# Kernel optimization log

Measured on AMD Instinct MI355X. Metric: run time of the kernel, lower is better.

The kernel has to match this reference:

```python
import jax, jax.numpy as jnp
import numpy as np

NUM_HEADS = 8


def setup_inputs() -> dict:
    B, S, D, Q, SEG = 4, 4096, 512, 1, 256
    key = jax.random.key(0)
    ks = jax.random.split(key, 7)
    x = jax.random.normal(ks[0], (B, S, D), dtype=jnp.float32)
    seg_id = jnp.sort(jax.random.randint(ks[1], (B, S), 0, SEG), axis=-1)
    # ensure every row actually spans segment ids 0..SEG-1 so max()+1 == SEG
    seg_id = seg_id.at[:, 0].set(0).at[:, -1].set(SEG - 1)
    valid_mask = jnp.ones((B, S), dtype=bool)
    query_bank = jax.random.normal(ks[2], (1, 1, Q, D), dtype=jnp.float32)
    scale = 0.02
    w_q = jax.random.normal(ks[3], (D, D), dtype=jnp.float32) * scale
    w_k = jax.random.normal(ks[4], (D, D), dtype=jnp.float32) * scale
    w_v = jax.random.normal(ks[5], (D, D), dtype=jnp.float32) * scale
    w_o = jax.random.normal(ks[6], (D, D), dtype=jnp.float32) * scale
    return {"x": x, "seg_id": seg_id, "valid_mask": valid_mask, "s_seg_max": SEG,
            "query_bank": query_bank, "w_q": w_q, "w_k": w_k, "w_v": w_v, "w_o": w_o}


def reference(x, seg_id, valid_mask, s_seg_max, query_bank, w_q, w_k, w_v, w_o):
    B, S, D = x.shape
    Q = query_bank.shape[2]
    H = NUM_HEADS
    hd = D // H
    L = s_seg_max * Q  # number of pooled queries

    # expand learned query bank over batch and segments, project (Linear: x @ W.T)
    queries = jnp.broadcast_to(query_bank, (B, s_seg_max, Q, D)).reshape(B, L, D)
    q = (queries @ w_q.T).reshape(B, L, H, hd).transpose(0, 2, 1, 3)   # bhqd
    k = (x @ w_k.T).reshape(B, S, H, hd).transpose(0, 2, 1, 3)         # bhkd
    v = (x @ w_v.T).reshape(B, S, H, hd).transpose(0, 2, 1, 3)         # bhkd

    # torch SDPA boolean mask semantics: True = participate in attention
    seg_for_query = jnp.repeat(jnp.arange(s_seg_max), Q)               # [L]
    attend = (seg_id[:, None, :] != seg_for_query[None, :, None]) | (~valid_mask[:, None, :])  # [B,L,S]

    scores = jnp.einsum('bhqd,bhkd->bhqk', q, k) / np.sqrt(hd).astype(x.dtype)
    scores = jnp.where(attend[:, None, :, :], scores, -jnp.inf)
    attn = jax.nn.softmax(scores, axis=-1)
    out = jnp.einsum('bhqk,bhkd->bhqd', attn, v)                       # [B,H,L,hd]
    out = out.transpose(0, 2, 1, 3).reshape(B, L, D)
    return out @ w_o.T
```

## Files before the change

kernel.cpp:

```cpp
#include <hip/hip_runtime.h>
#include <hip/hip_bf16.h>


#define S 4096
#define D 512
#define H 8
#define SEG 256
#define NROW 1024

typedef short bf16x8 __attribute__((ext_vector_type(8)));
typedef float fvec4  __attribute__((ext_vector_type(4)));

constexpr int OFF_SEGO   = 0;
constexpr int OFF_DSEG   = 1032;
constexpr int OFF_NALL   = 9224;
constexpr int OFF_C16    = 11272;
constexpr int OFF_PSEG_F = 15368;
constexpr int OFF_NSEG_F = 2112520;
constexpr size_t WS_FLOATS = 2374664;

static __device__ inline ushort f2bf(float f) {
    __hip_bfloat16 h = __float2bfloat16(f);
    return *reinterpret_cast<ushort*>(&h);
}
static __device__ inline float bf2f(ushort u) {
    return __uint_as_float(((uint)u) << 16);
}
static __device__ inline uint pack2(float a, float b) {
    return (uint)f2bf(a) | ((uint)f2bf(b) << 16);
}

__global__ __launch_bounds__(512) void k_setup(const float* __restrict__ qb,
        const float* __restrict__ w_q, const float* __restrict__ w_k,
        const int* __restrict__ seg_id, float* __restrict__ W) {
    int tid = threadIdx.x, blk = blockIdx.x;
    if (blk < 8) {
        __shared__ float qbs[D];
        __shared__ float part[64][9];
        __shared__ float qp[64];
        int h = blk;
        qbs[tid] = qb[tid];
        __syncthreads();
        int jj = tid >> 3, p = tid & 7;
        const float* wr = w_q + (size_t)(h*64 + jj)*D;
        float a = 0.f;
        for (int t = 0; t < 64; ++t) a += qbs[p + 8*t] * wr[p + 8*t];
        part[jj][p] = a;
        __syncthreads();
        if (tid < 64) {
            float s = 0.f;
            #pragma unroll
            for (int p2 = 0; p2 < 8; ++p2) s += part[tid][p2];
            qp[tid] = s;
        }
        __syncthreads();
        float c = 0.f;
        for (int j2 = 0; j2 < 64; ++j2)
            c += qp[j2] * w_k[(size_t)(h*64 + j2)*D + tid];
        ((ushort*)(W + OFF_C16))[h*512 + tid] = f2bf(c * 0.125f);
    } else if (blk < 12) {
        int b = blk - 8;
        if (tid <= SEG) {
            const int* sid = seg_id + (size_t)b*S;
            int lo = 0, hi = S;
            while (lo < hi) { int mid = (lo+hi) >> 1; if (sid[mid] < tid) lo = mid+1; else hi = mid; }
            ((int*)(W + OFF_SEGO))[b*(SEG+1) + tid] = lo;
        }
    } else {
        for (int t = tid; t < 4*D; t += 512) W[OFF_NALL + t] = 0.f;
        uint* c16u = (uint*)(W + OFF_C16);
        #pragma unroll
        for (int j = 0; j < 4; ++j) c16u[2048 + tid*4 + j] = 0u;
    }
}

__global__ __launch_bounds__(256) void k_pseg(const float* __restrict__ x,
                                              float* __restrict__ W) {
    __shared__ ushort xs[32][520];
    __shared__ ushort cls[16][520];
    __shared__ float E_lds[32][12];
    int row = blockIdx.x, b = row >> 8, l = row & 255, tid = threadIdx.x;
    const ushort* c16g = (const ushort*)(W + OFF_C16);
    #pragma unroll
    for (int rep = 0; rep < 4; ++rep) {
        int q = rep*256 + tid, r = q >> 6, c8 = q & 63;
        *(bf16x8*)&cls[r][c8*8] = *(const bf16x8*)&c16g[r*512 + c8*8];
    }
    const int* off = (const int*)(W + OFF_SEGO);
    int k0 = off[b*(SEG+1) + l], k1 = off[b*(SEG+1) + l + 1];
    float2 acc[8]; float es[8];
    #pragma unroll
    for (int h = 0; h < 8; ++h) { acc[h] = make_float2(0.f,0.f); es[h] = 0.f; }
    int lane = tid & 63, wave = tid >> 6;

    for (int kc = k0; kc < k1; kc += 32) {
        int nk = min(32, k1 - kc);
        __syncthreads();
        #pragma unroll
        for (int rep = 0; rep < 16; ++rep) {
            int t4 = rep*256 + tid, r = t4 >> 7, c4 = t4 & 127;
            if (r < nk) {
                float4 v = ((const float4*)(x + (size_t)(b*S + kc + r)*D))[c4];
                uint2 u; u.x = pack2(v.x, v.y); u.y = pack2(v.z, v.w);
                *(uint2*)&xs[r][c4*4] = u;
            }
        }
        __syncthreads();
        if (wave < 2 && wave*16 < nk) {
            int m = lane & 15, kg = lane >> 4;
            fvec4 sc = {0,0,0,0};
            for (int ks = 0; ks < 512; ks += 32) {
                bf16x8 a  = *(const bf16x8*)&xs[wave*16 + m][ks + kg*8];
                bf16x8 bb = *(const bf16x8*)&cls[m][ks + kg*8];
                sc = __builtin_amdgcn_mfma_f32_16x16x32_bf16(a, bb, sc, 0, 0, 0);
            }
            int h = m;
            #pragma unroll
            for (int r = 0; r < 4; ++r) {
                int kl = wave*16 + kg*4 + r;
                if (h < 8 && kl < nk) E_lds[kl][h] = __expf(sc[r]);
            }
        }
        __syncthreads();
        for (int kk = 0; kk < nk; ++kk) {
            uint xv = *(const uint*)&xs[kk][2*tid];
            float x0 = bf2f((ushort)(xv & 0xffff));
            float x1 = bf2f((ushort)(xv >> 16));
            float4 ea = *(const float4*)&E_lds[kk][0];
            float4 eb = *(const float4*)&E_lds[kk][4];
            float e[8] = {ea.x,ea.y,ea.z,ea.w,eb.x,eb.y,eb.z,eb.w};
            #pragma unroll
            for (int h = 0; h < 8; ++h) {
                acc[h].x += e[h]*x0;
                acc[h].y += e[h]*x1;
                es[h]    += e[h];
            }
        }
    }
    uint* Pb = (uint*)(W + OFF_PSEG_F);
    #pragma unroll
    for (int h = 0; h < 8; ++h)
        Pb[(size_t)row*2048 + h*256 + tid] = pack2(acc[h].x, acc[h].y);
    if (tid == 0) {
        #pragma unroll
        for (int h = 0; h < 8; ++h) W[OFF_DSEG + row*8 + h] = es[h];
    }
}

__global__ __launch_bounds__(256) void k_gemm_v(const float* __restrict__ w_v,
                                                float* __restrict__ W) {
    __shared__ ushort As[32][520];
    __shared__ ushort Bs[64][520];
    __shared__ float colsum[2][64];
    int rt = blockIdx.x, h = blockIdx.y, tid = threadIdx.x;
    const ushort* Pb = (const ushort*)(W + OFF_PSEG_F);
    #pragma unroll
    for (int rep = 0; rep < 8; ++rep) {
        int idx = rep*256 + tid, r = idx >> 6, j = idx & 63;
        *(bf16x8*)&As[r][j*8] =
            *(const bf16x8*)&Pb[(size_t)((rt*32 + r)*8 + h)*512 + j*8];
    }
    #pragma unroll
    for (int rep = 0; rep < 32; ++rep) {
        int idx = rep*256 + tid, r = idx >> 7, c4 = idx & 127;
        float4 v = ((const float4*)(w_v + (size_t)(h*64 + r)*512))[c4];
        uint2 u; u.x = pack2(v.x, v.y); u.y = pack2(v.z, v.w);
        *(uint2*)&Bs[r][c4*4] = u;
    }
    __syncthreads();
    int lane = tid & 63, w = tid >> 6;
    int wm = w & 1, wn = w >> 1;
    int m = lane & 15, kg = lane >> 4;
    fvec4 acc0 = {0,0,0,0}, acc1 = {0,0,0,0};
    for (int ks = 0; ks < 512; ks += 32) {
        bf16x8 a  = *(const bf16x8*)&As[wm*16 + m][ks + kg*8];
        bf16x8 b0 = *(const bf16x8*)&Bs[wn*32 + m][ks + kg*8];
        bf16x8 b1 = *(const bf16x8*)&Bs[wn*32 + 16 + m][ks + kg*8];
        acc0 = __builtin_amdgcn_mfma_f32_16x16x32_bf16(a, b0, acc0, 0, 0, 0);
        acc1 = __builtin_amdgcn_mfma_f32_16x16x32_bf16(a, b1, acc1, 0, 0, 0);
    }
    ushort* NSb = (ushort*)(W + OFF_NSEG_F);
    int rowbase = rt*32 + wm*16 + kg*4;
    int col0 = h*64 + wn*32 + m, col1 = col0 + 16;
    float s0 = 0.f, s1 = 0.f;
    #pragma unroll
    for (int r = 0; r < 4; ++r) {
        NSb[(size_t)(rowbase + r)*512 + col0] = f2bf(acc0[r]);
        NSb[(size_t)(rowbase + r)*512 + col1] = f2bf(acc1[r]);
        s0 += acc0[r]; s1 += acc1[r];
    }
    s0 += __shfl_xor(s0, 16); s0 += __shfl_xor(s0, 32);
    s1 += __shfl_xor(s1, 16); s1 += __shfl_xor(s1, 32);
    if (lane < 16) {
        colsum[wm][wn*32 + lane]      = s0;
        colsum[wm][wn*32 + 16 + lane] = s1;
    }
    __syncthreads();
    if (tid < 64) {
        int b = rt >> 3;
        atomicAdd(&W[OFF_NALL + b*512 + h*64 + tid], colsum[0][tid] + colsum[1][tid]);
    }
}

__global__ __launch_bounds__(256) void k_gemm_o(const float* __restrict__ w_o,
                                                float* __restrict__ W,
                                                float* __restrict__ out) {
    __shared__ ushort As[32][520];
    __shared__ ushort Bs[64][520];
    __shared__ float NAl[512];
    __shared__ float dpart[8][8];
    __shared__ float invs[32][8];
    int rt = blockIdx.x, nt = blockIdx.y, tid = threadIdx.x;
    int b = rt >> 3;
    if (tid < 64) {
        int h = tid >> 3, sg = tid & 7;
        float s = 0.f;
        for (int l2 = sg*32; l2 < sg*32 + 32; ++l2)
            s += W[OFF_DSEG + (b*256 + l2)*8 + h];
        dpart[h][sg] = s;
    }
    NAl[tid]       = W[OFF_NALL + b*512 + tid];
    NAl[tid + 256] = W[OFF_NALL + b*512 + tid + 256];
    __syncthreads();
    {
        int r = tid >> 3, h = tid & 7;
        float da = 0.f;
        #pragma unroll
        for (int sg = 0; sg < 8; ++sg) da += dpart[h][sg];
        invs[r][h] = 1.f / (da - W[OFF_DSEG + (rt*32 + r)*8 + h]);
    }
    #pragma unroll
    for (int rep = 0; rep < 32; ++rep) {
        int idx = rep*256 + tid, r = idx >> 7, c4 = idx & 127;
        float4 v = ((const float4*)(w_o + (size_t)(nt*64 + r)*512))[c4];
        uint2 u; u.x = pack2(v.x, v.y); u.y = pack2(v.z, v.w);
        *(uint2*)&Bs[r][c4*4] = u;
    }
    __syncthreads();
    const ushort* NSb = (const ushort*)(W + OFF_NSEG_F);
    #pragma unroll
    for (int rep = 0; rep < 8; ++rep) {
        int idx = rep*256 + tid, r = idx >> 6, j = idx & 63;
        bf16x8 ns = *(const bf16x8*)&NSb[(size_t)(rt*32 + r)*512 + j*8];
        float inv = invs[r][j >> 3];
        ushort o[8];
        #pragma unroll
        for (int e = 0; e < 8; ++e)
            o[e] = f2bf((NAl[j*8 + e] - bf2f((ushort)ns[e])) * inv);
        uint4 u;
        u.x = o[0] | ((uint)o[1] << 16);
        u.y = o[2] | ((uint)o[3] << 16);
        u.z = o[4] | ((uint)o[5] << 16);
        u.w = o[6] | ((uint)o[7] << 16);
        *(uint4*)&As[r][j*8] = u;
    }
    __syncthreads();
    int lane = tid & 63, w = tid >> 6;
    int wm = w & 1, wn = w >> 1;
    int m = lane & 15, kg = lane >> 4;
    fvec4 acc0 = {0,0,0,0}, acc1 = {0,0,0,0};
    for (int ks = 0; ks < 512; ks += 32) {
        bf16x8 a  = *(const bf16x8*)&As[wm*16 + m][ks + kg*8];
        bf16x8 b0 = *(const bf16x8*)&Bs[wn*32 + m][ks + kg*8];
        bf16x8 b1 = *(const bf16x8*)&Bs[wn*32 + 16 + m][ks + kg*8];
        acc0 = __builtin_amdgcn_mfma_f32_16x16x32_bf16(a, b0, acc0, 0, 0, 0);
        acc1 = __builtin_amdgcn_mfma_f32_16x16x32_bf16(a, b1, acc1, 0, 0, 0);
    }
    int rowb = rt*32 + wm*16 + kg*4;
    int col0 = nt*64 + wn*32 + m, col1 = col0 + 16;
    #pragma unroll
    for (int r = 0; r < 4; ++r) {
        out[(size_t)(rowb + r)*512 + col0] = acc0[r];
        out[(size_t)(rowb + r)*512 + col1] = acc1[r];
    }
}

extern "C" void kernel_launch(void* const* d_in, const int* in_sizes, int n_in,
                              void* d_out, int out_size, void* d_ws, size_t ws_size,
                              hipStream_t stream) {
    const float* x   = (const float*)d_in[0];
    const int*   seg = (const int*)d_in[1];
    const float* qb  = (const float*)d_in[4];
    const float* w_q = (const float*)d_in[5];
    const float* w_k = (const float*)d_in[6];
    const float* w_v = (const float*)d_in[7];
    const float* w_o = (const float*)d_in[8];
    float* W   = (float*)d_ws;
    float* out = (float*)d_out;

    if (ws_size < WS_FLOATS * sizeof(float)) return;

    hipLaunchKernelGGL(k_setup,  dim3(13),    dim3(512), 0, stream, qb, w_q, w_k, seg, W);
    hipLaunchKernelGGL(k_pseg,   dim3(NROW),  dim3(256), 0, stream, x, W);
    hipLaunchKernelGGL(k_gemm_v, dim3(32, 8), dim3(256), 0, stream, w_v, W);
    hipLaunchKernelGGL(k_gemm_o, dim3(32, 8), dim3(256), 0, stream, w_o, W, out);
}
```

Measured before the change: 37.60 us.

## Fuse four kernels into one cooperative persistent kernel with grid syncs

```diff
diff --git a/kernel.cpp b/kernel.cpp
--- a/kernel.cpp
+++ b/kernel.cpp
@@ -1,5 +1,8 @@
 #include <hip/hip_runtime.h>
 #include <hip/hip_bf16.h>
+#include <hip/hip_cooperative_groups.h>
+
+namespace cg = cooperative_groups;
 
 
 #define S 4096
@@ -28,6 +31,311 @@
 }
 static __device__ inline uint pack2(float a, float b) {
     return (uint)f2bf(a) | ((uint)f2bf(b) << 16);
+}
+
+__global__ __launch_bounds__(256, 1) void k_mega(
+        const float* __restrict__ x, const int* __restrict__ seg_id,
+        const float* __restrict__ qb, const float* __restrict__ w_q,
+        const float* __restrict__ w_k, const float* __restrict__ w_v,
+        const float* __restrict__ w_o, float* __restrict__ W,
+        float* __restrict__ out) {
+    cg::grid_group grid = cg::this_grid();
+    __shared__ __align__(16) char sm[54016];
+    int tid = threadIdx.x, blk = blockIdx.x;
+
+    if (blk < 8) {
+        float* qbs  = (float*)sm;
+        float* part = (float*)(sm + 2048);
+        float* qp   = (float*)(sm + 3328);
+        int h = blk;
+        qbs[tid] = qb[tid];
+        qbs[tid + 256] = qb[tid + 256];
+        __syncthreads();
+        int jj = tid >> 2, p = tid & 3;
+        const float* wr = w_q + (size_t)(h*64 + jj)*D;
+        float a = 0.f;
+        for (int t = 0; t < 128; ++t) a += qbs[p + 4*t] * wr[p + 4*t];
+        part[jj*5 + p] = a;
+        __syncthreads();
+        if (tid < 64) {
+            float s = part[tid*5] + part[tid*5+1] + part[tid*5+2] + part[tid*5+3];
+            qp[tid] = s;
+        }
+        __syncthreads();
+        ushort* c16 = (ushort*)(W + OFF_C16);
+        #pragma unroll
+        for (int half = 0; half < 2; ++half) {
+            int i = tid + half*256;
+            float c = 0.f;
+            for (int j2 = 0; j2 < 64; ++j2)
+                c += qp[j2] * w_k[(size_t)(h*64 + j2)*D + i];
+            c16[h*512 + i] = f2bf(c * 0.125f);
+        }
+    } else if (blk < 12) {
+        int b = blk - 8;
+        const int* sid = seg_id + (size_t)b*S;
+        int* offp = (int*)(W + OFF_SEGO);
+        int l = tid;
+        int lo = 0, hi = S;
+        while (lo < hi) { int mid = (lo+hi) >> 1; if (sid[mid] < l) lo = mid+1; else hi = mid; }
+        offp[b*257 + l] = lo;
+        if (tid == 0) offp[b*257 + 256] = S;
+    } else if (blk == 12) {
+        #pragma unroll
+        for (int j = 0; j < 8; ++j) W[OFF_NALL + tid*8 + j] = 0.f;
+        uint* c16u = (uint*)(W + OFF_C16);
+        #pragma unroll
+        for (int j = 0; j < 8; ++j) c16u[2048 + tid*8 + j] = 0u;
+    }
+    grid.sync();
+
+    {
+        ushort* xs  = (ushort*)sm;
+        ushort* cls = (ushort*)(sm + 33280);
+        float*  E   = (float*)(sm + 49920);
+        const ushort* c16g = (const ushort*)(W + OFF_C16);
+        #pragma unroll
+        for (int rep = 0; rep < 4; ++rep) {
+            int q = rep*256 + tid, r = q >> 6, c8 = q & 63;
+            *(bf16x8*)&cls[r*520 + c8*8] = *(const bf16x8*)&c16g[r*512 + c8*8];
+        }
+        int row0 = blk*4, b = blk >> 6, l0 = row0 & 255;
+        const int* offp = (const int*)(W + OFF_SEGO);
+        int ko0 = __builtin_amdgcn_readfirstlane(offp[b*257 + l0]);
+        int ko1 = __builtin_amdgcn_readfirstlane(offp[b*257 + l0 + 1]);
+        int ko2 = __builtin_amdgcn_readfirstlane(offp[b*257 + l0 + 2]);
+        int ko3 = __builtin_amdgcn_readfirstlane(offp[b*257 + l0 + 3]);
+        int k4  = __builtin_amdgcn_readfirstlane(offp[b*257 + l0 + 4]);
+        float2 acc[4][8]; float es_[4][8];
+        #pragma unroll
+        for (int s2 = 0; s2 < 4; ++s2)
+            #pragma unroll
+            for (int h = 0; h < 8; ++h) { acc[s2][h] = make_float2(0.f,0.f); es_[s2][h] = 0.f; }
+        int lane = tid & 63, wave = tid >> 6;
+        float4 pf[16];
+
+        int kc = ko0, nk = min(32, k4 - kc);
+        if (kc < k4) {
+            #pragma unroll
+            for (int rep = 0; rep < 16; ++rep) {
+                int t4 = rep*256 + tid, r = t4 >> 7, c4 = t4 & 127;
+                if (r < nk) pf[rep] = ((const float4*)(x + (size_t)(b*S + kc + r)*D))[c4];
+            }
+        }
+        while (kc < k4) {
+            __syncthreads();
+            #pragma unroll
+            for (int rep = 0; rep < 16; ++rep) {
+                int t4 = rep*256 + tid, r = t4 >> 7, c4 = t4 & 127;
+                if (r < nk) {
+                    float4 v = pf[rep];
+                    uint2 u; u.x = pack2(v.x, v.y); u.y = pack2(v.z, v.w);
+                    *(uint2*)&xs[r*520 + c4*4] = u;
+                }
+            }
+            __syncthreads();
+            int kcn = kc + 32;
+            int nkn = (kcn < k4) ? min(32, k4 - kcn) : 0;
+            if (nkn) {
+                #pragma unroll
+                for (int rep = 0; rep < 16; ++rep) {
+                    int t4 = rep*256 + tid, r = t4 >> 7, c4 = t4 & 127;
+                    if (r < nkn) pf[rep] = ((const float4*)(x + (size_t)(b*S + kcn + r)*D))[c4];
+                }
+            }
+            if (wave < 2 && wave*16 < nk) {
+                int m = lane & 15, kg = lane >> 4;
+                fvec4 sc = {0,0,0,0};
+                for (int ks = 0; ks < 512; ks += 32) {
+                    bf16x8 a  = *(const bf16x8*)&xs[(wave*16 + m)*520 + ks + kg*8];
+                    bf16x8 bb = *(const bf16x8*)&cls[m*520 + ks + kg*8];
+                    sc = __builtin_amdgcn_mfma_f32_16x16x32_bf16(a, bb, sc, 0, 0, 0);
+                }
+                #pragma unroll
+                for (int r = 0; r < 4; ++r) {
+                    int kl = wave*16 + kg*4 + r;
+                    if (m < 8 && kl < nk) E[kl*12 + m] = __expf(sc[r]);
+                }
+            }
+            __syncthreads();
+            #define ACCUM(sidx)                                             \
+                { _Pragma("unroll")                                         \
+                  for (int h = 0; h < 8; ++h) {                             \
+                      acc[sidx][h].x += e[h]*x0;                            \
+                      acc[sidx][h].y += e[h]*x1;                            \
+                      es_[sidx][h]   += e[h];                               \
+                  } }
+            for (int kk = 0; kk < nk; ++kk) {
+                uint xv = *(const uint*)&xs[kk*520 + 2*tid];
+                float x0 = bf2f((ushort)(xv & 0xffff));
+                float x1 = bf2f((ushort)(xv >> 16));
+                float4 ea = *(const float4*)&E[kk*12];
+                float4 eb = *(const float4*)&E[kk*12 + 4];
+                float e[8] = {ea.x,ea.y,ea.z,ea.w,eb.x,eb.y,eb.z,eb.w};
+                int key = kc + kk;
+                if (key < ko1)      ACCUM(0)
+                else if (key < ko2) ACCUM(1)
+                else if (key < ko3) ACCUM(2)
+                else                ACCUM(3)
+            }
+            #undef ACCUM
+            kc = kcn; nk = nkn;
+        }
+        uint* Pb = (uint*)(W + OFF_PSEG_F);
+        #pragma unroll
+        for (int rl = 0; rl < 4; ++rl)
+            #pragma unroll
+            for (int h = 0; h < 8; ++h)
+                Pb[(size_t)(row0 + rl)*2048 + h*256 + tid] =
+                    pack2(acc[rl][h].x, acc[rl][h].y);
+        if (tid == 0) {
+            #pragma unroll
+            for (int rl = 0; rl < 4; ++rl)
+                #pragma unroll
+                for (int h = 0; h < 8; ++h)
+                    W[OFF_DSEG + (row0 + rl)*8 + h] = es_[rl][h];
+        }
+    }
+    grid.sync();
+
+    {
+        int rt = blk & 31, h = blk >> 5;
+        ushort* As = (ushort*)sm;
+        ushort* Bs = (ushort*)(sm + 16896);
+        float* colsum = (float*)(sm + 50688);
+        const ushort* Pb = (const ushort*)(W + OFF_PSEG_F);
+        int lane = tid & 63, w = tid >> 6;
+        int wm = w & 1, wn = w >> 1;
+        int m = lane & 15, kg = lane >> 4;
+        fvec4 acc0 = {0,0,0,0}, acc1 = {0,0,0,0};
+        for (int kh = 0; kh < 2; ++kh) {
+            __syncthreads();
+            #pragma unroll
+            for (int rep = 0; rep < 4; ++rep) {
+                int idx = rep*256 + tid, r = idx >> 5, j8 = idx & 31;
+                *(bf16x8*)&As[r*264 + j8*8] =
+                    *(const bf16x8*)&Pb[(size_t)((rt*32 + r)*8 + h)*512 + kh*256 + j8*8];
+            }
+            #pragma unroll
+            for (int rep = 0; rep < 8; ++rep) {
+                int idx = rep*256 + tid, r = idx >> 5, j8 = idx & 31;
+                const float4* s4 = (const float4*)(w_v + (size_t)(h*64 + r)*512 + kh*256 + j8*8);
+                float4 v0 = s4[0], v1 = s4[1];
+                uint4 u;
+                u.x = pack2(v0.x, v0.y); u.y = pack2(v0.z, v0.w);
+                u.z = pack2(v1.x, v1.y); u.w = pack2(v1.z, v1.w);
+                *(uint4*)&Bs[r*264 + j8*8] = u;
+            }
+            __syncthreads();
+            #pragma unroll
+            for (int ks = 0; ks < 256; ks += 32) {
+                bf16x8 a  = *(const bf16x8*)&As[(wm*16 + m)*264 + ks + kg*8];
+                bf16x8 b0 = *(const bf16x8*)&Bs[(wn*32 + m)*264 + ks + kg*8];
+                bf16x8 b1 = *(const bf16x8*)&Bs[(wn*32 + 16 + m)*264 + ks + kg*8];
+                acc0 = __builtin_amdgcn_mfma_f32_16x16x32_bf16(a, b0, acc0, 0, 0, 0);
+                acc1 = __builtin_amdgcn_mfma_f32_16x16x32_bf16(a, b1, acc1, 0, 0, 0);
+            }
+        }
+        ushort* NSb = (ushort*)(W + OFF_NSEG_F);
+        int rowbase = rt*32 + wm*16 + kg*4;
+        int col0 = h*64 + wn*32 + m, col1 = col0 + 16;
+        float s0 = 0.f, s1 = 0.f;
+        #pragma unroll
+        for (int r = 0; r < 4; ++r) {
+            NSb[(size_t)(rowbase + r)*512 + col0] = f2bf(acc0[r]);
+            NSb[(size_t)(rowbase + r)*512 + col1] = f2bf(acc1[r]);
+            s0 += acc0[r]; s1 += acc1[r];
+        }
+        s0 += __shfl_xor(s0, 16); s0 += __shfl_xor(s0, 32);
+        s1 += __shfl_xor(s1, 16); s1 += __shfl_xor(s1, 32);
+        if (lane < 16) {
+            colsum[wm*64 + wn*32 + lane]      = s0;
+            colsum[wm*64 + wn*32 + 16 + lane] = s1;
+        }
+        __syncthreads();
+        if (tid < 64) {
+            int b = rt >> 3;
+            atomicAdd(&W[OFF_NALL + b*512 + h*64 + tid], colsum[tid] + colsum[64 + tid]);
+        }
+    }
+    grid.sync();
+
+    {
+        int rt = blk & 31, nt = blk >> 5, b = rt >> 3;
+        ushort* As   = (ushort*)sm;
+        ushort* Bs   = (ushort*)(sm + 16896);
+        float* NAl   = (float*)(sm + 50688);
+        float* dpart = (float*)(sm + 52736);
+        float* invs  = (float*)(sm + 52992);
+        if (tid < 64) {
+            int h = tid >> 3, sg = tid & 7;
+            float s = 0.f;
+            for (int l2 = sg*32; l2 < sg*32 + 32; ++l2)
+                s += W[OFF_DSEG + (b*256 + l2)*8 + h];
+            dpart[h*8 + sg] = s;
+        }
+        NAl[tid]       = W[OFF_NALL + b*512 + tid];
+        NAl[tid + 256] = W[OFF_NALL + b*512 + tid + 256];
+        __syncthreads();
+        {
+            int r = tid >> 3, h = tid & 7;
+            float da = 0.f;
+            #pragma unroll
+            for (int sg = 0; sg < 8; ++sg) da += dpart[h*8 + sg];
+            invs[r*8 + h] = 1.f / (da - W[OFF_DSEG + (rt*32 + r)*8 + h]);
+        }
+        const ushort* NSb = (const ushort*)(W + OFF_NSEG_F);
+        int lane = tid & 63, w = tid >> 6;
+        int wm = w & 1, wn = w >> 1;
+        int m = lane & 15, kg = lane >> 4;
+        fvec4 acc0 = {0,0,0,0}, acc1 = {0,0,0,0};
+        for (int kh = 0; kh < 2; ++kh) {
+            __syncthreads();
+            #pragma unroll
+            for (int rep = 0; rep < 4; ++rep) {
+                int idx = rep*256 + tid, r = idx >> 5, j8 = idx & 31;
+                int jc = kh*256 + j8*8;
+                bf16x8 ns = *(const bf16x8*)&NSb[(size_t)(rt*32 + r)*512 + jc];
+                float inv = invs[r*8 + (jc >> 6)];
+                ushort o[8];
+                #pragma unroll
+                for (int e = 0; e < 8; ++e)
+                    o[e] = f2bf((NAl[jc + e] - bf2f((ushort)ns[e])) * inv);
+                uint4 u;
+                u.x = o[0] | ((uint)o[1] << 16);
+                u.y = o[2] | ((uint)o[3] << 16);
+                u.z = o[4] | ((uint)o[5] << 16);
+                u.w = o[6] | ((uint)o[7] << 16);
+                *(uint4*)&As[r*264 + j8*8] = u;
+            }
+            #pragma unroll
+            for (int rep = 0; rep < 8; ++rep) {
+                int idx = rep*256 + tid, r = idx >> 5, j8 = idx & 31;
+                const float4* s4 = (const float4*)(w_o + (size_t)(nt*64 + r)*512 + kh*256 + j8*8);
+                float4 v0 = s4[0], v1 = s4[1];
+                uint4 u;
+                u.x = pack2(v0.x, v0.y); u.y = pack2(v0.z, v0.w);
+                u.z = pack2(v1.x, v1.y); u.w = pack2(v1.z, v1.w);
+                *(uint4*)&Bs[r*264 + j8*8] = u;
+            }
+            __syncthreads();
+            #pragma unroll
+            for (int ks = 0; ks < 256; ks += 32) {
+                bf16x8 a  = *(const bf16x8*)&As[(wm*16 + m)*264 + ks + kg*8];
+                bf16x8 b0 = *(const bf16x8*)&Bs[(wn*32 + m)*264 + ks + kg*8];
+                bf16x8 b1 = *(const bf16x8*)&Bs[(wn*32 + 16 + m)*264 + ks + kg*8];
+                acc0 = __builtin_amdgcn_mfma_f32_16x16x32_bf16(a, b0, acc0, 0, 0, 0);
+                acc1 = __builtin_amdgcn_mfma_f32_16x16x32_bf16(a, b1, acc1, 0, 0, 0);
+            }
+        }
+        int rowb = rt*32 + wm*16 + kg*4;
+        int col0 = nt*64 + wn*32 + m, col1 = col0 + 16;
+        #pragma unroll
+        for (int r = 0; r < 4; ++r) {
+            out[(size_t)(rowb + r)*512 + col0] = acc0[r];
+            out[(size_t)(rowb + r)*512 + col1] = acc1[r];
+        }
+    }
 }
 
 __global__ __launch_bounds__(512) void k_setup(const float* __restrict__ qb,
@@ -92,7 +400,6 @@
     #pragma unroll
     for (int h = 0; h < 8; ++h) { acc[h] = make_float2(0.f,0.f); es[h] = 0.f; }
     int lane = tid & 63, wave = tid >> 6;
-
     for (int kc = k0; kc < k1; kc += 32) {
         int nk = min(32, k1 - kc);
         __syncthreads();
@@ -114,11 +421,10 @@
                 bf16x8 bb = *(const bf16x8*)&cls[m][ks + kg*8];
                 sc = __builtin_amdgcn_mfma_f32_16x16x32_bf16(a, bb, sc, 0, 0, 0);
             }
-            int h = m;
             #pragma unroll
             for (int r = 0; r < 4; ++r) {
                 int kl = wave*16 + kg*4 + r;
-                if (h < 8 && kl < nk) E_lds[kl][h] = __expf(sc[r]);
+                if (m < 8 && kl < nk) E_lds[kl][m] = __expf(sc[r]);
             }
         }
         __syncthreads();
@@ -290,8 +596,15 @@
 
     if (ws_size < WS_FLOATS * sizeof(float)) return;
 
-    hipLaunchKernelGGL(k_setup,  dim3(13),    dim3(512), 0, stream, qb, w_q, w_k, seg, W);
-    hipLaunchKernelGGL(k_pseg,   dim3(NROW),  dim3(256), 0, stream, x, W);
-    hipLaunchKernelGGL(k_gemm_v, dim3(32, 8), dim3(256), 0, stream, w_v, W);
-    hipLaunchKernelGGL(k_gemm_o, dim3(32, 8), dim3(256), 0, stream, w_o, W, out);
-}
+    void* args[] = {(void*)&x, (void*)&seg, (void*)&qb, (void*)&w_q, (void*)&w_k,
+                    (void*)&w_v, (void*)&w_o, (void*)&W, (void*)&out};
+    hipError_t e = hipLaunchCooperativeKernel((const void*)k_mega, dim3(256),
+                                              dim3(256), args, 0, stream);
+    if (e != hipSuccess) {
+        (void)hipGetLastError();
+        hipLaunchKernelGGL(k_setup,  dim3(13),    dim3(512), 0, stream, qb, w_q, w_k, seg, W);
+        hipLaunchKernelGGL(k_pseg,   dim3(NROW),  dim3(256), 0, stream, x, W);
+        hipLaunchKernelGGL(k_gemm_v, dim3(32, 8), dim3(256), 0, stream, w_v, W);
+        hipLaunchKernelGGL(k_gemm_o, dim3(32, 8), dim3(256), 0, stream, w_o, W, out);
+    }
+}
```

Result: slower. 139.2 us (+270.3%).

## Fuse segment pooling with V projection, four segments per block, prefetch x

Applied to the files above, without the earlier changes.

```diff
diff --git a/kernel.cpp b/kernel.cpp
--- a/kernel.cpp
+++ b/kernel.cpp
@@ -6,18 +6,18 @@
 #define D 512
 #define H 8
 #define SEG 256
-#define NROW 1024
 
 typedef short bf16x8 __attribute__((ext_vector_type(8)));
 typedef float fvec4  __attribute__((ext_vector_type(4)));
+typedef float f32x2  __attribute__((ext_vector_type(2)));
 
 constexpr int OFF_SEGO   = 0;
 constexpr int OFF_DSEG   = 1032;
 constexpr int OFF_NALL   = 9224;
 constexpr int OFF_C16    = 11272;
-constexpr int OFF_PSEG_F = 15368;
-constexpr int OFF_NSEG_F = 2112520;
-constexpr size_t WS_FLOATS = 2374664;
+constexpr int OFF_NSEG_F = 15368;
+constexpr int OFF_WVB_F  = 277512;
+constexpr size_t WS_FLOATS = 408584;
 
 static __device__ inline ushort f2bf(float f) {
     __hip_bfloat16 h = __float2bfloat16(f);
@@ -32,7 +32,8 @@
 
 __global__ __launch_bounds__(512) void k_setup(const float* __restrict__ qb,
         const float* __restrict__ w_q, const float* __restrict__ w_k,
-        const int* __restrict__ seg_id, float* __restrict__ W) {
+        const float* __restrict__ w_v, const int* __restrict__ seg_id,
+        float* __restrict__ W) {
     int tid = threadIdx.x, blk = blockIdx.x;
     if (blk < 8) {
         __shared__ float qbs[D];
@@ -66,139 +67,173 @@
             while (lo < hi) { int mid = (lo+hi) >> 1; if (sid[mid] < tid) lo = mid+1; else hi = mid; }
             ((int*)(W + OFF_SEGO))[b*(SEG+1) + tid] = lo;
         }
-    } else {
+    } else if (blk == 12) {
         for (int t = tid; t < 4*D; t += 512) W[OFF_NALL + t] = 0.f;
         uint* c16u = (uint*)(W + OFF_C16);
         #pragma unroll
         for (int j = 0; j < 4; ++j) c16u[2048 + tid*4 + j] = 0u;
-    }
-}
-
-__global__ __launch_bounds__(256) void k_pseg(const float* __restrict__ x,
-                                              float* __restrict__ W) {
-    __shared__ ushort xs[32][520];
-    __shared__ ushort cls[16][520];
-    __shared__ float E_lds[32][12];
-    int row = blockIdx.x, b = row >> 8, l = row & 255, tid = threadIdx.x;
+    } else {
+        ushort* dst = (ushort*)(W + OFF_WVB_F);
+        int base = (blk - 13) * 8192;
+        #pragma unroll
+        for (int rep = 0; rep < 2; ++rep) {
+            int idx = base + rep*4096 + tid*8;
+            const float4* s4 = (const float4*)(w_v + idx);
+            float4 v0 = s4[0], v1 = s4[1];
+            uint4 u;
+            u.x = pack2(v0.x, v0.y); u.y = pack2(v0.z, v0.w);
+            u.z = pack2(v1.x, v1.y); u.w = pack2(v1.z, v1.w);
+            *(uint4*)&dst[idx] = u;
+        }
+    }
+}
+
+__global__ __launch_bounds__(256) void k_psegv(const float* __restrict__ x,
+                                               float* __restrict__ W) {
+    __shared__ __align__(16) char sm[51456];
+    int tid = threadIdx.x, blk = blockIdx.x;
+    int lane = tid & 63, wave = tid >> 6;
+    int row0 = blk*4, b = blk >> 6, l0 = row0 & 255;
+
+    ushort* xs  = (ushort*)sm;
+    ushort* cls = (ushort*)(sm + 33280);
+    float*  E   = (float*)(sm + 49920);
     const ushort* c16g = (const ushort*)(W + OFF_C16);
     #pragma unroll
     for (int rep = 0; rep < 4; ++rep) {
         int q = rep*256 + tid, r = q >> 6, c8 = q & 63;
-        *(bf16x8*)&cls[r][c8*8] = *(const bf16x8*)&c16g[r*512 + c8*8];
-    }
-    const int* off = (const int*)(W + OFF_SEGO);
-    int k0 = off[b*(SEG+1) + l], k1 = off[b*(SEG+1) + l + 1];
-    float2 acc[8]; float es[8];
-    #pragma unroll
-    for (int h = 0; h < 8; ++h) { acc[h] = make_float2(0.f,0.f); es[h] = 0.f; }
-    int lane = tid & 63, wave = tid >> 6;
-
-    for (int kc = k0; kc < k1; kc += 32) {
-        int nk = min(32, k1 - kc);
+        *(bf16x8*)&cls[r*520 + c8*8] = *(const bf16x8*)&c16g[r*512 + c8*8];
+    }
+    const int* offp = (const int*)(W + OFF_SEGO);
+    int ko0 = __builtin_amdgcn_readfirstlane(offp[b*257 + l0]);
+    int ko1 = __builtin_amdgcn_readfirstlane(offp[b*257 + l0 + 1]);
+    int ko2 = __builtin_amdgcn_readfirstlane(offp[b*257 + l0 + 2]);
+    int ko3 = __builtin_amdgcn_readfirstlane(offp[b*257 + l0 + 3]);
+    int k4  = __builtin_amdgcn_readfirstlane(offp[b*257 + l0 + 4]);
+    f32x2 acc[4][8]; f32x2 es2[4][4];
+    #pragma unroll
+    for (int s2 = 0; s2 < 4; ++s2) {
+        #pragma unroll
+        for (int h = 0; h < 8; ++h) acc[s2][h] = f32x2{0.f, 0.f};
+        #pragma unroll
+        for (int h = 0; h < 4; ++h) es2[s2][h] = f32x2{0.f, 0.f};
+    }
+    float4 pf[16];
+    int kc = ko0, nk = min(32, k4 - kc);
+    if (kc < k4) {
+        #pragma unroll
+        for (int rep = 0; rep < 16; ++rep) {
+            int t4 = rep*256 + tid, r = t4 >> 7, c4 = t4 & 127;
+            if (r < nk) pf[rep] = ((const float4*)(x + (size_t)(b*S + kc + r)*D))[c4];
+        }
+    }
+    while (kc < k4) {
         __syncthreads();
         #pragma unroll
         for (int rep = 0; rep < 16; ++rep) {
             int t4 = rep*256 + tid, r = t4 >> 7, c4 = t4 & 127;
             if (r < nk) {
-                float4 v = ((const float4*)(x + (size_t)(b*S + kc + r)*D))[c4];
+                float4 v = pf[rep];
                 uint2 u; u.x = pack2(v.x, v.y); u.y = pack2(v.z, v.w);
-                *(uint2*)&xs[r][c4*4] = u;
-            }
-        }
-        __syncthreads();
+                *(uint2*)&xs[r*520 + c4*4] = u;
+            }
+        }
+        __syncthreads();
+        int kcn = kc + 32;
+        int nkn = (kcn < k4) ? min(32, k4 - kcn) : 0;
+        if (nkn) {
+            #pragma unroll
+            for (int rep = 0; rep < 16; ++rep) {
+                int t4 = rep*256 + tid, r = t4 >> 7, c4 = t4 & 127;
+                if (r < nkn) pf[rep] = ((const float4*)(x + (size_t)(b*S + kcn + r)*D))[c4];
+            }
+        }
         if (wave < 2 && wave*16 < nk) {
             int m = lane & 15, kg = lane >> 4;
             fvec4 sc = {0,0,0,0};
             for (int ks = 0; ks < 512; ks += 32) {
-                bf16x8 a  = *(const bf16x8*)&xs[wave*16 + m][ks + kg*8];
-                bf16x8 bb = *(const bf16x8*)&cls[m][ks + kg*8];
+                bf16x8 a  = *(const bf16x8*)&xs[(wave*16 + m)*520 + ks + kg*8];
+                bf16x8 bb = *(const bf16x8*)&cls[m*520 + ks + kg*8];
                 sc = __builtin_amdgcn_mfma_f32_16x16x32_bf16(a, bb, sc, 0, 0, 0);
             }
-            int h = m;
             #pragma unroll
             for (int r = 0; r < 4; ++r) {
                 int kl = wave*16 + kg*4 + r;
-                if (h < 8 && kl < nk) E_lds[kl][h] = __expf(sc[r]);
-            }
-        }
-        __syncthreads();
+                if (m < 8 && kl < nk) E[kl*12 + m] = __expf(sc[r]);
+            }
+        }
+        __syncthreads();
+        #define ACCUM(sidx)                                             \
+            { _Pragma("unroll")                                         \
+              for (int h = 0; h < 8; ++h) acc[sidx][h] += e[h]*x01;     \
+              _Pragma("unroll")                                         \
+              for (int hp = 0; hp < 4; ++hp) es2[sidx][hp] += epair[hp]; }
         for (int kk = 0; kk < nk; ++kk) {
-            uint xv = *(const uint*)&xs[kk][2*tid];
-            float x0 = bf2f((ushort)(xv & 0xffff));
-            float x1 = bf2f((ushort)(xv >> 16));
-            float4 ea = *(const float4*)&E_lds[kk][0];
-            float4 eb = *(const float4*)&E_lds[kk][4];
+            uint xv = *(const uint*)&xs[kk*520 + 2*tid];
+            f32x2 x01;
+            x01[0] = bf2f((ushort)(xv & 0xffff));
+            x01[1] = bf2f((ushort)(xv >> 16));
+            float4 ea = *(const float4*)&E[kk*12];
+            float4 eb = *(const float4*)&E[kk*12 + 4];
             float e[8] = {ea.x,ea.y,ea.z,ea.w,eb.x,eb.y,eb.z,eb.w};
-            #pragma unroll
-            for (int h = 0; h < 8; ++h) {
-                acc[h].x += e[h]*x0;
-                acc[h].y += e[h]*x1;
-                es[h]    += e[h];
-            }
-        }
-    }
-    uint* Pb = (uint*)(W + OFF_PSEG_F);
-    #pragma unroll
-    for (int h = 0; h < 8; ++h)
-        Pb[(size_t)row*2048 + h*256 + tid] = pack2(acc[h].x, acc[h].y);
+            f32x2 epair[4];
+            epair[0] = f32x2{ea.x, ea.y}; epair[1] = f32x2{ea.z, ea.w};
+            epair[2] = f32x2{eb.x, eb.y}; epair[3] = f32x2{eb.z, eb.w};
+            int key = kc + kk;
+            if (key < ko1)      ACCUM(0)
+            else if (key < ko2) ACCUM(1)
+            else if (key < ko3) ACCUM(2)
+            else                ACCUM(3)
+        }
+        #undef ACCUM
+        kc = kcn; nk = nkn;
+    }
+
+    __syncthreads();
+    ushort* A_lds = (ushort*)sm;
+    #pragma unroll
+    for (int rl = 0; rl < 4; ++rl)
+        #pragma unroll
+        for (int h = 0; h < 8; ++h)
+            *(uint*)&A_lds[(h*4 + rl)*520 + 2*tid] = pack2(acc[rl][h][0], acc[rl][h][1]);
     if (tid == 0) {
         #pragma unroll
-        for (int h = 0; h < 8; ++h) W[OFF_DSEG + row*8 + h] = es[h];
-    }
-}
-
-__global__ __launch_bounds__(256) void k_gemm_v(const float* __restrict__ w_v,
-                                                float* __restrict__ W) {
-    __shared__ ushort As[32][520];
-    __shared__ ushort Bs[64][520];
-    __shared__ float colsum[2][64];
-    int rt = blockIdx.x, h = blockIdx.y, tid = threadIdx.x;
-    const ushort* Pb = (const ushort*)(W + OFF_PSEG_F);
-    #pragma unroll
-    for (int rep = 0; rep < 8; ++rep) {
-        int idx = rep*256 + tid, r = idx >> 6, j = idx & 63;
-        *(bf16x8*)&As[r][j*8] =
-            *(const bf16x8*)&Pb[(size_t)((rt*32 + r)*8 + h)*512 + j*8];
-    }
-    #pragma unroll
-    for (int rep = 0; rep < 32; ++rep) {
-        int idx = rep*256 + tid, r = idx >> 7, c4 = idx & 127;
-        float4 v = ((const float4*)(w_v + (size_t)(h*64 + r)*512))[c4];
-        uint2 u; u.x = pack2(v.x, v.y); u.y = pack2(v.z, v.w);
-        *(uint2*)&Bs[r][c4*4] = u;
-    }
-    __syncthreads();
-    int lane = tid & 63, w = tid >> 6;
-    int wm = w & 1, wn = w >> 1;
+        for (int rl = 0; rl < 4; ++rl)
+            #pragma unroll
+            for (int h = 0; h < 8; ++h)
+                W[OFF_DSEG + (row0 + rl)*8 + h] = es2[rl][h>>1][h&1];
+    }
+    __syncthreads();
+    ushort* Bs = (ushort*)(sm + 33280);
+    const ushort* wvb = (const ushort*)(W + OFF_WVB_F);
+    ushort* NSb = (ushort*)(W + OFF_NSEG_F);
     int m = lane & 15, kg = lane >> 4;
-    fvec4 acc0 = {0,0,0,0}, acc1 = {0,0,0,0};
-    for (int ks = 0; ks < 512; ks += 32) {
-        bf16x8 a  = *(const bf16x8*)&As[wm*16 + m][ks + kg*8];
-        bf16x8 b0 = *(const bf16x8*)&Bs[wn*32 + m][ks + kg*8];
-        bf16x8 b1 = *(const bf16x8*)&Bs[wn*32 + 16 + m][ks + kg*8];
-        acc0 = __builtin_amdgcn_mfma_f32_16x16x32_bf16(a, b0, acc0, 0, 0, 0);
-        acc1 = __builtin_amdgcn_mfma_f32_16x16x32_bf16(a, b1, acc1, 0, 0, 0);
-    }
-    ushort* NSb = (ushort*)(W + OFF_NSEG_F);
-    int rowbase = rt*32 + wm*16 + kg*4;
-    int col0 = h*64 + wn*32 + m, col1 = col0 + 16;
-    float s0 = 0.f, s1 = 0.f;
-    #pragma unroll
-    for (int r = 0; r < 4; ++r) {
-        NSb[(size_t)(rowbase + r)*512 + col0] = f2bf(acc0[r]);
-        NSb[(size_t)(rowbase + r)*512 + col1] = f2bf(acc1[r]);
-        s0 += acc0[r]; s1 += acc1[r];
-    }
-    s0 += __shfl_xor(s0, 16); s0 += __shfl_xor(s0, 32);
-    s1 += __shfl_xor(s1, 16); s1 += __shfl_xor(s1, 32);
-    if (lane < 16) {
-        colsum[wm][wn*32 + lane]      = s0;
-        colsum[wm][wn*32 + 16 + lane] = s1;
-    }
-    __syncthreads();
-    if (tid < 64) {
-        int b = rt >> 3;
-        atomicAdd(&W[OFF_NALL + b*512 + h*64 + tid], colsum[0][tid] + colsum[1][tid]);
+    for (int h = 0; h < 8; ++h) {
+        fvec4 an = {0,0,0,0};
+        for (int kchunk = 0; kchunk < 4; ++kchunk) {
+            __syncthreads();
+            #pragma unroll
+            for (int rep = 0; rep < 4; ++rep) {
+                int idx = rep*256 + tid, r = idx >> 4, c8 = idx & 15;
+                *(bf16x8*)&Bs[r*136 + c8*8] =
+                    *(const bf16x8*)&wvb[(size_t)(h*64 + r)*512 + kchunk*128 + c8*8];
+            }
+            __syncthreads();
+            #pragma unroll
+            for (int ks = 0; ks < 128; ks += 32) {
+                bf16x8 a  = *(const bf16x8*)&A_lds[(h*4 + (m & 3))*520 + kchunk*128 + ks + kg*8];
+                bf16x8 bb = *(const bf16x8*)&Bs[(wave*16 + m)*136 + ks + kg*8];
+                an = __builtin_amdgcn_mfma_f32_16x16x32_bf16(a, bb, an, 0, 0, 0);
+            }
+        }
+        if (lane < 16) {
+            int col = h*64 + wave*16 + lane;
+            float s = an[0] + an[1] + an[2] + an[3];
+            #pragma unroll
+            for (int r = 0; r < 4; ++r)
+                NSb[(size_t)(row0 + r)*512 + col] = f2bf(an[r]);
+            atomicAdd(&W[OFF_NALL + b*512 + col], s);
+        }
     }
 }
 
@@ -290,8 +325,7 @@
 
     if (ws_size < WS_FLOATS * sizeof(float)) return;
 
-    hipLaunchKernelGGL(k_setup,  dim3(13),    dim3(512), 0, stream, qb, w_q, w_k, seg, W);
-    hipLaunchKernelGGL(k_pseg,   dim3(NROW),  dim3(256), 0, stream, x, W);
-    hipLaunchKernelGGL(k_gemm_v, dim3(32, 8), dim3(256), 0, stream, w_v, W);
+    hipLaunchKernelGGL(k_setup,  dim3(45),    dim3(512), 0, stream, qb, w_q, w_k, w_v, seg, W);
+    hipLaunchKernelGGL(k_psegv,  dim3(256),   dim3(256), 0, stream, x, W);
     hipLaunchKernelGGL(k_gemm_o, dim3(32, 8), dim3(256), 0, stream, w_o, W, out);
 }
```

New measurement: 69.57 us. 85.0% more time.

## Project all keys through W_v before segment pooling instead of after

Applied to the files above, without the earlier changes.

```diff
diff --git a/kernel.cpp b/kernel.cpp
--- a/kernel.cpp
+++ b/kernel.cpp
@@ -6,18 +6,18 @@
 #define D 512
 #define H 8
 #define SEG 256
-#define NROW 1024
 
 typedef short bf16x8 __attribute__((ext_vector_type(8)));
 typedef float fvec4  __attribute__((ext_vector_type(4)));
 
-constexpr int OFF_SEGO   = 0;
-constexpr int OFF_DSEG   = 1032;
-constexpr int OFF_NALL   = 9224;
-constexpr int OFF_C16    = 11272;
-constexpr int OFF_PSEG_F = 15368;
-constexpr int OFF_NSEG_F = 2112520;
-constexpr size_t WS_FLOATS = 2374664;
+constexpr int    OFF_SEGO   = 0;
+constexpr int    OFF_DSEG   = 1032;
+constexpr int    OFF_NALL   = 9224;
+constexpr int    OFF_E_F    = 11272;
+constexpr int    OFF_V_F    = 76808;
+constexpr int    OFF_NSEG_F = 4271112;
+constexpr int    OFF_BAUG_F = 4533256;
+constexpr size_t WS_FLOATS  = 4680712;
 
 static __device__ inline ushort f2bf(float f) {
     __hip_bfloat16 h = __float2bfloat16(f);
@@ -32,8 +32,10 @@
 
 __global__ __launch_bounds__(512) void k_setup(const float* __restrict__ qb,
         const float* __restrict__ w_q, const float* __restrict__ w_k,
-        const int* __restrict__ seg_id, float* __restrict__ W) {
+        const float* __restrict__ w_v, const int* __restrict__ seg_id,
+        float* __restrict__ W) {
     int tid = threadIdx.x, blk = blockIdx.x;
+    ushort* baug = (ushort*)(W + OFF_BAUG_F);
     if (blk < 8) {
         __shared__ float qbs[D];
         __shared__ float part[64][9];
@@ -57,7 +59,7 @@
         float c = 0.f;
         for (int j2 = 0; j2 < 64; ++j2)
             c += qp[j2] * w_k[(size_t)(h*64 + j2)*D + tid];
-        ((ushort*)(W + OFF_C16))[h*512 + tid] = f2bf(c * 0.125f);
+        baug[(size_t)(512 + h)*512 + tid] = f2bf(c * 0.125f);
     } else if (blk < 12) {
         int b = blk - 8;
         if (tid <= SEG) {
@@ -66,140 +68,99 @@
             while (lo < hi) { int mid = (lo+hi) >> 1; if (sid[mid] < tid) lo = mid+1; else hi = mid; }
             ((int*)(W + OFF_SEGO))[b*(SEG+1) + tid] = lo;
         }
+    } else if (blk == 12) {
+        for (int t = tid; t < 4*D; t += 512) W[OFF_NALL + t] = 0.f;
+        uint* pB = (uint*)baug;
+        for (int t = tid; t < 14336; t += 512) pB[133120 + t] = 0u;
     } else {
-        for (int t = tid; t < 4*D; t += 512) W[OFF_NALL + t] = 0.f;
-        uint* c16u = (uint*)(W + OFF_C16);
-        #pragma unroll
-        for (int j = 0; j < 4; ++j) c16u[2048 + tid*4 + j] = 0u;
-    }
-}
-
-__global__ __launch_bounds__(256) void k_pseg(const float* __restrict__ x,
-                                              float* __restrict__ W) {
-    __shared__ ushort xs[32][520];
-    __shared__ ushort cls[16][520];
-    __shared__ float E_lds[32][12];
-    int row = blockIdx.x, b = row >> 8, l = row & 255, tid = threadIdx.x;
-    const ushort* c16g = (const ushort*)(W + OFF_C16);
-    #pragma unroll
-    for (int rep = 0; rep < 4; ++rep) {
-        int q = rep*256 + tid, r = q >> 6, c8 = q & 63;
-        *(bf16x8*)&cls[r][c8*8] = *(const bf16x8*)&c16g[r*512 + c8*8];
-    }
-    const int* off = (const int*)(W + OFF_SEGO);
-    int k0 = off[b*(SEG+1) + l], k1 = off[b*(SEG+1) + l + 1];
-    float2 acc[8]; float es[8];
-    #pragma unroll
-    for (int h = 0; h < 8; ++h) { acc[h] = make_float2(0.f,0.f); es[h] = 0.f; }
-    int lane = tid & 63, wave = tid >> 6;
-
-    for (int kc = k0; kc < k1; kc += 32) {
-        int nk = min(32, k1 - kc);
-        __syncthreads();
-        #pragma unroll
-        for (int rep = 0; rep < 16; ++rep) {
-            int t4 = rep*256 + tid, r = t4 >> 7, c4 = t4 & 127;
-            if (r < nk) {
-                float4 v = ((const float4*)(x + (size_t)(b*S + kc + r)*D))[c4];
-                uint2 u; u.x = pack2(v.x, v.y); u.y = pack2(v.z, v.w);
-                *(uint2*)&xs[r][c4*4] = u;
-            }
-        }
-        __syncthreads();
-        if (wave < 2 && wave*16 < nk) {
-            int m = lane & 15, kg = lane >> 4;
-            fvec4 sc = {0,0,0,0};
-            for (int ks = 0; ks < 512; ks += 32) {
-                bf16x8 a  = *(const bf16x8*)&xs[wave*16 + m][ks + kg*8];
-                bf16x8 bb = *(const bf16x8*)&cls[m][ks + kg*8];
-                sc = __builtin_amdgcn_mfma_f32_16x16x32_bf16(a, bb, sc, 0, 0, 0);
-            }
-            int h = m;
-            #pragma unroll
-            for (int r = 0; r < 4; ++r) {
-                int kl = wave*16 + kg*4 + r;
-                if (h < 8 && kl < nk) E_lds[kl][h] = __expf(sc[r]);
-            }
-        }
-        __syncthreads();
-        for (int kk = 0; kk < nk; ++kk) {
-            uint xv = *(const uint*)&xs[kk][2*tid];
-            float x0 = bf2f((ushort)(xv & 0xffff));
-            float x1 = bf2f((ushort)(xv >> 16));
-            float4 ea = *(const float4*)&E_lds[kk][0];
-            float4 eb = *(const float4*)&E_lds[kk][4];
-            float e[8] = {ea.x,ea.y,ea.z,ea.w,eb.x,eb.y,eb.z,eb.w};
-            #pragma unroll
-            for (int h = 0; h < 8; ++h) {
-                acc[h].x += e[h]*x0;
-                acc[h].y += e[h]*x1;
-                es[h]    += e[h];
-            }
-        }
-    }
-    uint* Pb = (uint*)(W + OFF_PSEG_F);
-    #pragma unroll
-    for (int h = 0; h < 8; ++h)
-        Pb[(size_t)row*2048 + h*256 + tid] = pack2(acc[h].x, acc[h].y);
-    if (tid == 0) {
-        #pragma unroll
-        for (int h = 0; h < 8; ++h) W[OFF_DSEG + row*8 + h] = es[h];
-    }
-}
-
-__global__ __launch_bounds__(256) void k_gemm_v(const float* __restrict__ w_v,
-                                                float* __restrict__ W) {
-    __shared__ ushort As[32][520];
-    __shared__ ushort Bs[64][520];
-    __shared__ float colsum[2][64];
-    int rt = blockIdx.x, h = blockIdx.y, tid = threadIdx.x;
-    const ushort* Pb = (const ushort*)(W + OFF_PSEG_F);
-    #pragma unroll
-    for (int rep = 0; rep < 8; ++rep) {
-        int idx = rep*256 + tid, r = idx >> 6, j = idx & 63;
-        *(bf16x8*)&As[r][j*8] =
-            *(const bf16x8*)&Pb[(size_t)((rt*32 + r)*8 + h)*512 + j*8];
-    }
-    #pragma unroll
-    for (int rep = 0; rep < 32; ++rep) {
-        int idx = rep*256 + tid, r = idx >> 7, c4 = idx & 127;
-        float4 v = ((const float4*)(w_v + (size_t)(h*64 + r)*512))[c4];
-        uint2 u; u.x = pack2(v.x, v.y); u.y = pack2(v.z, v.w);
-        *(uint2*)&Bs[r][c4*4] = u;
-    }
-    __syncthreads();
+        int base = (blk - 13) * 8192;
+        #pragma unroll
+        for (int rep = 0; rep < 2; ++rep) {
+            int idx = base + rep*4096 + tid*8;
+            const float4* s4 = (const float4*)(w_v + idx);
+            float4 v0 = s4[0], v1 = s4[1];
+            uint4 u;
+            u.x = pack2(v0.x, v0.y); u.y = pack2(v0.z, v0.w);
+            u.z = pack2(v1.x, v1.y); u.w = pack2(v1.z, v1.w);
+            *(uint4*)&baug[idx] = u;
+        }
+    }
+}
+
+__global__ __launch_bounds__(256) void k_ev(const float* __restrict__ x,
+                                            float* __restrict__ W) {
+    __shared__ ushort As[32][136];
+    __shared__ ushort Bs[64][136];
+    int rt = blockIdx.x, nt = blockIdx.y, tid = threadIdx.x;
+    const ushort* baug = (const ushort*)(W + OFF_BAUG_F);
     int lane = tid & 63, w = tid >> 6;
     int wm = w & 1, wn = w >> 1;
     int m = lane & 15, kg = lane >> 4;
     fvec4 acc0 = {0,0,0,0}, acc1 = {0,0,0,0};
-    for (int ks = 0; ks < 512; ks += 32) {
-        bf16x8 a  = *(const bf16x8*)&As[wm*16 + m][ks + kg*8];
-        bf16x8 b0 = *(const bf16x8*)&Bs[wn*32 + m][ks + kg*8];
-        bf16x8 b1 = *(const bf16x8*)&Bs[wn*32 + 16 + m][ks + kg*8];
-        acc0 = __builtin_amdgcn_mfma_f32_16x16x32_bf16(a, b0, acc0, 0, 0, 0);
-        acc1 = __builtin_amdgcn_mfma_f32_16x16x32_bf16(a, b1, acc1, 0, 0, 0);
+    for (int kc = 0; kc < 4; ++kc) {
+        __syncthreads();
+        #pragma unroll
+        for (int rep = 0; rep < 4; ++rep) {
+            int idx = rep*256 + tid, r = idx >> 5, c4 = idx & 31;
+            float4 v = *(const float4*)(x + (size_t)(rt*32 + r)*512 + kc*128 + c4*4);
+            uint2 u; u.x = pack2(v.x, v.y); u.y = pack2(v.z, v.w);
+            *(uint2*)&As[r][c4*4] = u;
+        }
+        #pragma unroll
+        for (int rep = 0; rep < 4; ++rep) {
+            int idx = rep*256 + tid, r = idx >> 4, c8 = idx & 15;
+            *(bf16x8*)&Bs[r][c8*8] =
+                *(const bf16x8*)&baug[(size_t)(nt*64 + r)*512 + kc*128 + c8*8];
+        }
+        __syncthreads();
+        #pragma unroll
+        for (int ks = 0; ks < 128; ks += 32) {
+            bf16x8 a  = *(const bf16x8*)&As[wm*16 + m][ks + kg*8];
+            bf16x8 b0 = *(const bf16x8*)&Bs[wn*32 + m][ks + kg*8];
+            bf16x8 b1 = *(const bf16x8*)&Bs[wn*32 + 16 + m][ks + kg*8];
+            acc0 = __builtin_amdgcn_mfma_f32_16x16x32_bf16(a, b0, acc0, 0, 0, 0);
+            acc1 = __builtin_amdgcn_mfma_f32_16x16x32_bf16(a, b1, acc1, 0, 0, 0);
+        }
+    }
+    int rowb = rt*32 + wm*16 + kg*4;
+    if (nt < 8) {
+        ushort* vb = (ushort*)(W + OFF_V_F);
+        int col0 = nt*64 + wn*32 + m, col1 = col0 + 16;
+        #pragma unroll
+        for (int r = 0; r < 4; ++r) {
+            vb[(size_t)(rowb + r)*512 + col0] = f2bf(acc0[r]);
+            vb[(size_t)(rowb + r)*512 + col1] = f2bf(acc1[r]);
+        }
+    } else if (wn == 0 && m < 8) {
+        ushort* Eb = (ushort*)(W + OFF_E_F);
+        #pragma unroll
+        for (int r = 0; r < 4; ++r)
+            Eb[(size_t)(rowb + r)*8 + m] = f2bf(__expf(acc0[r]));
+    }
+}
+
+__global__ __launch_bounds__(256) void k_nseg(float* __restrict__ W) {
+    int row = blockIdx.x, b = row >> 8, l = row & 255, tid = threadIdx.x;
+    const int* offp = (const int*)(W + OFF_SEGO);
+    int k0 = __builtin_amdgcn_readfirstlane(offp[b*257 + l]);
+    int k1 = __builtin_amdgcn_readfirstlane(offp[b*257 + l + 1]);
+    const ushort* vb = (const ushort*)(W + OFF_V_F);
+    const ushort* Eb = (const ushort*)(W + OFF_E_F);
+    int h = tid >> 5;
+    float acc0 = 0.f, acc1 = 0.f, es = 0.f;
+    for (int k = k0; k < k1; ++k) {
+        size_t key = (size_t)(b*S + k);
+        float e = bf2f(Eb[key*8 + h]);
+        uint vv = *(const uint*)&vb[key*512 + 2*tid];
+        acc0 += e * bf2f((ushort)(vv & 0xffff));
+        acc1 += e * bf2f((ushort)(vv >> 16));
+        es   += e;
     }
     ushort* NSb = (ushort*)(W + OFF_NSEG_F);
-    int rowbase = rt*32 + wm*16 + kg*4;
-    int col0 = h*64 + wn*32 + m, col1 = col0 + 16;
-    float s0 = 0.f, s1 = 0.f;
-    #pragma unroll
-    for (int r = 0; r < 4; ++r) {
-        NSb[(size_t)(rowbase + r)*512 + col0] = f2bf(acc0[r]);
-        NSb[(size_t)(rowbase + r)*512 + col1] = f2bf(acc1[r]);
-        s0 += acc0[r]; s1 += acc1[r];
-    }
-    s0 += __shfl_xor(s0, 16); s0 += __shfl_xor(s0, 32);
-    s1 += __shfl_xor(s1, 16); s1 += __shfl_xor(s1, 32);
-    if (lane < 16) {
-        colsum[wm][wn*32 + lane]      = s0;
-        colsum[wm][wn*32 + 16 + lane] = s1;
-    }
-    __syncthreads();
-    if (tid < 64) {
-        int b = rt >> 3;
-        atomicAdd(&W[OFF_NALL + b*512 + h*64 + tid], colsum[0][tid] + colsum[1][tid]);
-    }
+    *(uint*)&NSb[(size_t)row*512 + 2*tid] = pack2(acc0, acc1);
+    atomicAdd(&W[OFF_NALL + b*512 + 2*tid],     acc0);
+    atomicAdd(&W[OFF_NALL + b*512 + 2*tid + 1], acc1);
+    if ((tid & 31) == 0) W[OFF_DSEG + row*8 + h] = es;
 }
 
 __global__ __launch_bounds__(256) void k_gemm_o(const float* __restrict__ w_o,
@@ -290,8 +251,8 @@
 
     if (ws_size < WS_FLOATS * sizeof(float)) return;
 
-    hipLaunchKernelGGL(k_setup,  dim3(13),    dim3(512), 0, stream, qb, w_q, w_k, seg, W);
-    hipLaunchKernelGGL(k_pseg,   dim3(NROW),  dim3(256), 0, stream, x, W);
-    hipLaunchKernelGGL(k_gemm_v, dim3(32, 8), dim3(256), 0, stream, w_v, W);
-    hipLaunchKernelGGL(k_gemm_o, dim3(32, 8), dim3(256), 0, stream, w_o, W, out);
-}
+    hipLaunchKernelGGL(k_setup,  dim3(45),     dim3(512), 0, stream, qb, w_q, w_k, w_v, seg, W);
+    hipLaunchKernelGGL(k_ev,     dim3(512, 9), dim3(256), 0, stream, x, W);
+    hipLaunchKernelGGL(k_nseg,   dim3(1024),   dim3(256), 0, stream, W);
+    hipLaunchKernelGGL(k_gemm_o, dim3(32, 8),  dim3(256), 0, stream, w_o, W, out);
+}
```

After: 73.23 us. +94.8%, slower.
